# Kernel optimization log

Hardware: AMD Instinct MI355X
Metric: run time of the kernel (lower is better)

## Reference

```python
import jax, jax.numpy as jnp
import numpy as np

B, C, CI, H, W = 8, 256, 128, 64, 64
EPS = 1e-5

def conv1x1(x, w, b):
    # x: [B,C,H,W], w: [O,C], b: [O]
    return jnp.einsum('bchw,oc->bohw', x, w) + b[None, :, None, None]

def avgpool2(x):
    b, c, h, w = x.shape
    return x.reshape(b, c, h // 2, 2, w // 2, 2).mean(axis=(3, 5))

def setup_inputs() -> dict:
    key = jax.random.key(0)
    ks = jax.random.split(key, 16)
    s = lambda fan: 1.0 / np.sqrt(fan)
    inp = {
        'q': jax.random.normal(ks[0], (B, C, H, W), jnp.float32),
        'k': jax.random.normal(ks[1], (B, C, H, W), jnp.float32),
        'v': jax.random.normal(ks[2], (B, C, H, W), jnp.float32),
        'Wg':  jax.random.normal(ks[3], (CI, C), jnp.float32) * s(C),
        'bg':  jax.random.normal(ks[4], (CI,), jnp.float32) * s(C),
        'Wth': jax.random.normal(ks[5], (CI, C), jnp.float32) * s(C),
        'bth': jax.random.normal(ks[6], (CI,), jnp.float32) * s(C),
        'Wph': jax.random.normal(ks[7], (CI, C), jnp.float32) * s(C),
        'bph': jax.random.normal(ks[8], (CI,), jnp.float32) * s(C),
        'Ww':  jax.random.normal(ks[9], (C, CI), jnp.float32) * s(CI),
        'bw':  jax.random.normal(ks[10], (C,), jnp.float32) * s(CI),
        'gamma': jax.random.normal(ks[11], (C,), jnp.float32) * 0.1 + 1.0,
        'beta':  jax.random.normal(ks[12], (C,), jnp.float32) * 0.1,
        'mean':  jax.random.normal(ks[13], (C,), jnp.float32) * 0.1,
        'var':   jax.random.uniform(ks[14], (C,), jnp.float32, 0.5, 1.5),
    }
    return inp

def reference(q, k, v, Wg, bg, Wth, bth, Wph, bph, Ww, bw, gamma, beta, mean, var):
    b = q.shape[0]
    # g branch on v, phi branch on q: 1x1 conv then 2x2 avg-pool (sub_sample)
    g_x = avgpool2(conv1x1(v, Wg, bg)).reshape(b, CI, -1)            # [B,CI,M]
    g_x = g_x.transpose(0, 2, 1)                                      # [B,M,CI]
    theta_x = conv1x1(k, Wth, bth).reshape(b, CI, -1).transpose(0, 2, 1)  # [B,N,CI]
    phi_x = avgpool2(conv1x1(q, Wph, bph)).reshape(b, CI, -1)        # [B,CI,M]
    f = jnp.einsum('bnc,bcm->bnm', theta_x, phi_x)                   # [B,N,M]
    f_div_C = jax.nn.softmax(f, axis=-1)
    y = jnp.einsum('bnm,bmc->bnc', f_div_C, g_x)                     # [B,N,CI]
    y = y.transpose(0, 2, 1).reshape(b, CI, H, W)
    W_y = conv1x1(y, Ww, bw)
    # BatchNorm2d (inference form)
    W_y = (W_y - mean[None, :, None, None]) * (gamma[None, :, None, None]
            * jax.lax.rsqrt(var + EPS)[None, :, None, None]) + beta[None, :, None, None]
    return W_y + v
```

## Files before the change

kernel.cpp:

```cpp
#include <hip/hip_runtime.h>
#include <cstddef>

typedef unsigned short u16;
typedef unsigned int u32;
typedef __attribute__((ext_vector_type(8))) __bf16 bf16x8;
typedef __attribute__((ext_vector_type(4))) float f32x4;

constexpr int kB = 8, kC = 256, kCI = 128, kN = 4096, kM = 1024;
constexpr float kEPS = 1e-5f;

__device__ __forceinline__ u16 f2bf(float f) {
    u32 u = __float_as_uint(f);
    u32 r = (u + 0x7fffu + ((u >> 16) & 1u)) >> 16;
    return (u16)r;
}

__global__ __launch_bounds__(256) void prep_kernel(const float* __restrict__ Wth,
                                                   const float* __restrict__ Wph,
                                                   const float* __restrict__ Wg,
                                                   const float* __restrict__ Ww,
                                                   const float* __restrict__ bw,
                                                   const float* __restrict__ gamma,
                                                   const float* __restrict__ beta,
                                                   const float* __restrict__ mean,
                                                   const float* __restrict__ var,
                                                   u16* __restrict__ Wthb,
                                                   u16* __restrict__ Wphb,
                                                   u16* __restrict__ Wgb,
                                                   u16* __restrict__ Wwsb,
                                                   float* __restrict__ bb) {
    int idx = blockIdx.x * 256 + threadIdx.x;
    if (idx < 32768) {
        Wthb[idx] = f2bf(Wth[idx]);
    } else if (idx < 65536) {
        int j = idx - 32768; Wphb[j] = f2bf(Wph[j]);
    } else if (idx < 98304) {
        int j = idx - 65536; Wgb[j] = f2bf(Wg[j]);
    } else {
        int j = idx - 98304;
        int co = j >> 7;
        float sc = gamma[co] * rsqrtf(var[co] + kEPS);
        Wwsb[j] = f2bf(Ww[j] * sc);
        if ((j & 127) == 0) bb[co] = (bw[co] - mean[co]) * sc + beta[co];
    }
}

template <int CMAJOR, int POOL>
__global__ __launch_bounds__(256) void convp_kernel(const float* __restrict__ x,
                                                    const u16* __restrict__ Wb,
                                                    const float* __restrict__ bias,
                                                    u16* __restrict__ out, int Mn) {
    __shared__ __align__(16) u16 w_lds[128 * 72];
    __shared__ __align__(16) u16 x_lds[64 * 64];
    int t = threadIdx.x, b = blockIdx.y, n0 = blockIdx.x * 64;
    int w = t >> 6, lane = t & 63, l15 = lane & 15, quad = lane >> 4;
    int xn = t & 63, cbb = (t >> 6) * 2;

    f32x4 acc[8];
#pragma unroll
    for (int i = 0; i < 8; i++) acc[i] = (f32x4){0.f, 0.f, 0.f, 0.f};

    for (int c0 = 0; c0 < kC; c0 += 64) {
        __syncthreads();
#pragma unroll
        for (int i = 0; i < 4; i++) {
            int u = t + 256 * i;
            int ci = u >> 3, blk = u & 7;
            *(uint4*)&w_lds[ci * 72 + blk * 8] =
                *(const uint4*)&Wb[ci * kC + c0 + blk * 8];
        }
#pragma unroll
        for (int cc = 0; cc < 2; cc++) {
            int cb = cbb + cc;
            float f[8];
            if (POOL) {
                int p = n0 + xn, ph_ = p >> 5, pw_ = p & 31;
#pragma unroll
                for (int j = 0; j < 8; j++) {
                    const float* src = x + ((size_t)(b * kC + c0 + cb * 8 + j) * 64
                                            + 2 * ph_) * 64 + 2 * pw_;
                    float2 a = *(const float2*)src;
                    float2 b2 = *(const float2*)(src + 64);
                    f[j] = 0.25f * (a.x + a.y + b2.x + b2.y);
                }
            } else {
#pragma unroll
                for (int j = 0; j < 8; j++)
                    f[j] = x[(size_t)(b * kC + c0 + cb * 8 + j) * Mn + n0 + xn];
            }
            uint4 pk;
            pk.x = (u32)f2bf(f[0]) | ((u32)f2bf(f[1]) << 16);
            pk.y = (u32)f2bf(f[2]) | ((u32)f2bf(f[3]) << 16);
            pk.z = (u32)f2bf(f[4]) | ((u32)f2bf(f[5]) << 16);
            pk.w = (u32)f2bf(f[6]) | ((u32)f2bf(f[7]) << 16);
            *(uint4*)&x_lds[xn * 64 + ((cb ^ (xn & 7)) * 8)] = pk;
        }
        __syncthreads();

#pragma unroll
        for (int ks = 0; ks < 2; ks++) {
            int px = w * 16 + l15;
            bf16x8 xf = *(const bf16x8*)&x_lds[px * 64 + (((ks * 4 + quad) ^ (px & 7)) * 8)];
#pragma unroll
            for (int ct = 0; ct < 8; ct++) {
                bf16x8 wf = *(const bf16x8*)&w_lds[(ct * 16 + l15) * 72 + ks * 32 + quad * 8];
                if (CMAJOR)
                    acc[ct] = __builtin_amdgcn_mfma_f32_16x16x32_bf16(xf, wf, acc[ct], 0, 0, 0);
                else
                    acc[ct] = __builtin_amdgcn_mfma_f32_16x16x32_bf16(wf, xf, acc[ct], 0, 0, 0);
            }
        }
    }

    if (CMAJOR == 0) {
        int px = n0 + w * 16 + l15;
#pragma unroll
        for (int ct = 0; ct < 8; ct++) {
            int ci0 = ct * 16 + quad * 4;
            uint2 pk;
            pk.x = (u32)f2bf(acc[ct][0] + bias[ci0 + 0]) |
                   ((u32)f2bf(acc[ct][1] + bias[ci0 + 1]) << 16);
            pk.y = (u32)f2bf(acc[ct][2] + bias[ci0 + 2]) |
                   ((u32)f2bf(acc[ct][3] + bias[ci0 + 3]) << 16);
            *(uint2*)&out[(size_t)(b * Mn + px) * kCI + ci0] = pk;
        }
    } else {
        int px = n0 + w * 16 + quad * 4;
#pragma unroll
        for (int ct = 0; ct < 8; ct++) {
            int ci = ct * 16 + l15;
            float bs = bias[ci];
            uint2 pk;
            pk.x = (u32)f2bf(acc[ct][0] + bs) | ((u32)f2bf(acc[ct][1] + bs) << 16);
            pk.y = (u32)f2bf(acc[ct][2] + bs) | ((u32)f2bf(acc[ct][3] + bs) << 16);
            *(uint2*)&out[(size_t)(b * kCI + ci) * Mn + px] = pk;
        }
    }
}

__global__ __launch_bounds__(128) void attn_kernel(const u16* __restrict__ theta,
                                                   const u16* __restrict__ phi,
                                                   const u16* __restrict__ g,
                                                   u16* __restrict__ y) {
    __shared__ __align__(16) u16 ph_lds[8192];
    __shared__ __align__(16) u16 g_lds[8192];
    __shared__ __align__(16) u16 p_lds[4096];

    int t = threadIdx.x, b = blockIdx.y, n0 = blockIdx.x * 64;
    int w = t >> 6, lane = t & 63, l15 = lane & 15, quad = lane >> 4;

    bf16x8 thf[2][4];
    const u16* thB = theta + ((size_t)(b * kN) + n0 + w * 32) * kCI;
#pragma unroll
    for (int nt = 0; nt < 2; nt++)
#pragma unroll
        for (int ks = 0; ks < 4; ks++)
            thf[nt][ks] = *(const bf16x8*)&thB[(size_t)(nt * 16 + l15) * kCI + ks * 32 + quad * 8];

    f32x4 oacc[8][2];
#pragma unroll
    for (int ct = 0; ct < 8; ct++) {
        oacc[ct][0] = (f32x4){0.f, 0.f, 0.f, 0.f};
        oacc[ct][1] = (f32x4){0.f, 0.f, 0.f, 0.f};
    }
    float m_[2] = {-1e30f, -1e30f}, l_[2] = {0.f, 0.f};

    const u16* phB = phi + (size_t)b * kM * kCI;
    const u16* gB  = g   + (size_t)b * kCI * kM;
    u16* pw = p_lds + w * 2048;

    for (int c0 = 0; c0 < kM; c0 += 64) {
        __syncthreads();
#pragma unroll
        for (int it = 0; it < 8; it++) {
            int u = t + 128 * it;
            int row = u >> 4, cb = u & 15;
            *(uint4*)&ph_lds[(cb >> 2) * 2048 + row * 32 + (cb & 3) * 8] =
                *(const uint4*)&phB[(size_t)(c0 + row) * kCI + cb * 8];
        }
#pragma unroll
        for (int it = 0; it < 8; it++) {
            int u = t + 128 * it;
            int ci = u >> 3, mb = u & 7;
            *(uint4*)&g_lds[(mb >> 2) * 4096 + ci * 32 + (mb & 3) * 8] =
                *(const uint4*)&gB[(size_t)ci * kM + c0 + mb * 8];
        }
        __syncthreads();

        f32x4 sacc[4][2];
#pragma unroll
        for (int mt = 0; mt < 4; mt++) {
            sacc[mt][0] = (f32x4){0.f, 0.f, 0.f, 0.f};
            sacc[mt][1] = (f32x4){0.f, 0.f, 0.f, 0.f};
        }
#pragma unroll
        for (int ks = 0; ks < 4; ks++)
#pragma unroll
            for (int mt = 0; mt < 4; mt++) {
                bf16x8 a = *(const bf16x8*)&ph_lds[ks * 2048 + (mt * 16 + l15) * 32 + quad * 8];
                sacc[mt][0] = __builtin_amdgcn_mfma_f32_16x16x32_bf16(a, thf[0][ks], sacc[mt][0], 0, 0, 0);
                sacc[mt][1] = __builtin_amdgcn_mfma_f32_16x16x32_bf16(a, thf[1][ks], sacc[mt][1], 0, 0, 0);
            }

#pragma unroll
        for (int nt = 0; nt < 2; nt++) {
            float mc = -1e30f;
#pragma unroll
            for (int mt = 0; mt < 4; mt++)
#pragma unroll
                for (int r = 0; r < 4; r++) mc = fmaxf(mc, sacc[mt][nt][r]);
            mc = fmaxf(mc, __shfl_xor(mc, 16, 64));
            mc = fmaxf(mc, __shfl_xor(mc, 32, 64));
            float mp = m_[nt];
            float mn = fmaxf(mp, mc);
            int resc = __any(mn != mp);
            float alpha = __expf(mp - mn);
            m_[nt] = mn;
            float rs = 0.f;
#pragma unroll
            for (int mt = 0; mt < 4; mt++)
#pragma unroll
                for (int r = 0; r < 4; r++) {
                    float p = __expf(sacc[mt][nt][r] - mn);
                    sacc[mt][nt][r] = p;
                    rs += p;
                }
            rs += __shfl_xor(rs, 16, 64);
            rs += __shfl_xor(rs, 32, 64);
            l_[nt] = l_[nt] * alpha + rs;
            if (resc) {
#pragma unroll
                for (int ct = 0; ct < 8; ct++)
#pragma unroll
                    for (int r = 0; r < 4; r++) oacc[ct][nt][r] *= alpha;
            }
#pragma unroll
            for (int mt = 0; mt < 4; mt++)
#pragma unroll
                for (int h = 0; h < 2; h++) {
                    u32 ue = __float_as_uint(sacc[mt][nt][2 * h]) + 0x8000u;
                    u32 uo = __float_as_uint(sacc[mt][nt][2 * h + 1]) + 0x8000u;
                    u32 d = (ue >> 16) | (uo & 0xffff0000u);
                    int m = mt * 16 + quad * 4 + 2 * h;
                    int off = ((m >> 5) * 2 + nt) * 512 + (((m >> 3) & 3) * 16 + l15) * 8 + (m & 7);
                    *(u32*)&pw[off] = d;
                }
        }

#pragma unroll
        for (int ks2 = 0; ks2 < 2; ks2++) {
            bf16x8 b0 = *(const bf16x8*)&pw[(ks2 * 2 + 0) * 512 + (quad * 16 + l15) * 8];
            bf16x8 b1 = *(const bf16x8*)&pw[(ks2 * 2 + 1) * 512 + (quad * 16 + l15) * 8];
#pragma unroll
            for (int ct = 0; ct < 8; ct++) {
                bf16x8 a = *(const bf16x8*)&g_lds[ks2 * 4096 + (ct * 16 + l15) * 32 + quad * 8];
                oacc[ct][0] = __builtin_amdgcn_mfma_f32_16x16x32_bf16(a, b0, oacc[ct][0], 0, 0, 0);
                oacc[ct][1] = __builtin_amdgcn_mfma_f32_16x16x32_bf16(a, b1, oacc[ct][1], 0, 0, 0);
            }
        }
    }

#pragma unroll
    for (int nt = 0; nt < 2; nt++) {
        float inv = 1.0f / l_[nt];
        int n = n0 + w * 32 + nt * 16 + l15;
        u16* yr = y + ((size_t)(b * kN) + n) * kCI + quad * 4;
#pragma unroll
        for (int ct = 0; ct < 8; ct++) {
            uint2 pk;
            pk.x = (u32)f2bf(oacc[ct][nt][0] * inv) | ((u32)f2bf(oacc[ct][nt][1] * inv) << 16);
            pk.y = (u32)f2bf(oacc[ct][nt][2] * inv) | ((u32)f2bf(oacc[ct][nt][3] * inv) << 16);
            *(uint2*)&yr[ct * 16] = pk;
        }
    }
}

__global__ __launch_bounds__(256) void final_kernel(const u16* __restrict__ y,
                                                    const u16* __restrict__ Wws,
                                                    const float* __restrict__ bb,
                                                    const float* __restrict__ v,
                                                    float* __restrict__ out) {
    __shared__ __align__(16) u16 y_lds[64 * 136];
    int t = threadIdx.x, b = blockIdx.y, n0 = blockIdx.x * 64;
    int w = t >> 6, lane = t & 63, l15 = lane & 15, quad = lane >> 4;

#pragma unroll
    for (int i = 0; i < 4; i++) {
        int u = t + 256 * i;
        int row = u >> 4, blk = u & 15;
        *(uint4*)&y_lds[row * 136 + blk * 8] =
            *(const uint4*)&y[(size_t)(b * kN + n0 + row) * kCI + blk * 8];
    }
    __syncthreads();

    bf16x8 af[4];
#pragma unroll
    for (int ks = 0; ks < 4; ks++)
        af[ks] = *(const bf16x8*)&y_lds[(w * 16 + l15) * 136 + ks * 32 + quad * 8];

#pragma unroll
    for (int ct = 0; ct < 16; ct++) {
        f32x4 a = (f32x4){0.f, 0.f, 0.f, 0.f};
#pragma unroll
        for (int ks = 0; ks < 4; ks++) {
            bf16x8 bf = *(const bf16x8*)&Wws[(ct * 16 + l15) * kCI + ks * 32 + quad * 8];
            a = __builtin_amdgcn_mfma_f32_16x16x32_bf16(af[ks], bf, a, 0, 0, 0);
        }
        int co = ct * 16 + l15;
        float bbv = bb[co];
        size_t base = (size_t)(b * kC + co) * kN + n0 + w * 16 + quad * 4;
        float4 vv = *(const float4*)&v[base];
        float4 ov;
        ov.x = a[0] + bbv + vv.x;
        ov.y = a[1] + bbv + vv.y;
        ov.z = a[2] + bbv + vv.z;
        ov.w = a[3] + bbv + vv.w;
        *(float4*)&out[base] = ov;
    }
}

extern "C" void kernel_launch(void* const* d_in, const int* in_sizes, int n_in,
                              void* d_out, int out_size, void* d_ws, size_t ws_size,
                              hipStream_t stream) {
    (void)in_sizes; (void)n_in; (void)out_size; (void)ws_size;
    const float* q     = (const float*)d_in[0];
    const float* k     = (const float*)d_in[1];
    const float* v     = (const float*)d_in[2];
    const float* Wg    = (const float*)d_in[3];
    const float* bg    = (const float*)d_in[4];
    const float* Wth   = (const float*)d_in[5];
    const float* bth   = (const float*)d_in[6];
    const float* Wph   = (const float*)d_in[7];
    const float* bph   = (const float*)d_in[8];
    const float* Ww    = (const float*)d_in[9];
    const float* bw    = (const float*)d_in[10];
    const float* gamma = (const float*)d_in[11];
    const float* beta  = (const float*)d_in[12];
    const float* mean  = (const float*)d_in[13];
    const float* var   = (const float*)d_in[14];
    float* out = (float*)d_out;

    u16* wsu = (u16*)d_ws;
    u16*   theta = wsu;
    u16*   phi   = theta + 4194304;
    u16*   gbuf  = phi + 1048576;
    u16*   ybuf  = gbuf + 1048576;
    u16*   Wthb  = ybuf + 4194304;
    u16*   Wphb  = Wthb + 32768;
    u16*   Wgb   = Wphb + 32768;
    u16*   Wwsb  = Wgb + 32768;
    float* bbuf  = (float*)(Wwsb + 32768);

    prep_kernel<<<dim3(512), 256, 0, stream>>>(Wth, Wph, Wg, Ww, bw, gamma, beta,
                                               mean, var, Wthb, Wphb, Wgb, Wwsb, bbuf);
    convp_kernel<0, 0><<<dim3(64, 8), 256, 0, stream>>>(k, Wthb, bth, theta, kN);
    convp_kernel<0, 1><<<dim3(16, 8), 256, 0, stream>>>(q, Wphb, bph, phi, kM);
    convp_kernel<1, 1><<<dim3(16, 8), 256, 0, stream>>>(v, Wgb, bg, gbuf, kM);
    attn_kernel<<<dim3(64, 8), 128, 0, stream>>>(theta, phi, gbuf, ybuf);
    final_kernel<<<dim3(64, 8), 256, 0, stream>>>(ybuf, Wwsb, bbuf, v, out);
}
```

Measured before the change: 270.8 us.

## Merge conv launches, drop LDS staging in attention and final kernels

After: 260.3 us. 1.04x faster.

```diff
diff --git a/kernel.cpp b/kernel.cpp
--- a/kernel.cpp
+++ b/kernel.cpp
@@ -45,14 +45,14 @@
     }
 }
 
-template <int CMAJOR, int POOL>
-__global__ __launch_bounds__(256) void convp_kernel(const float* __restrict__ x,
-                                                    const u16* __restrict__ Wb,
-                                                    const float* __restrict__ bias,
-                                                    u16* __restrict__ out, int Mn) {
-    __shared__ __align__(16) u16 w_lds[128 * 72];
-    __shared__ __align__(16) u16 x_lds[64 * 64];
-    int t = threadIdx.x, b = blockIdx.y, n0 = blockIdx.x * 64;
+template <int POOL>
+__device__ __forceinline__ void conv_body(const float* __restrict__ x,
+                                          const u16* __restrict__ Wb,
+                                          const float* __restrict__ bias,
+                                          u16* __restrict__ out, int Mn,
+                                          int cmajor, int b, int n0,
+                                          u16* w_lds, u16* x_lds) {
+    int t = threadIdx.x;
     int w = t >> 6, lane = t & 63, l15 = lane & 15, quad = lane >> 4;
     int xn = t & 63, cbb = (t >> 6) * 2;
 
@@ -104,7 +104,7 @@
 #pragma unroll
             for (int ct = 0; ct < 8; ct++) {
                 bf16x8 wf = *(const bf16x8*)&w_lds[(ct * 16 + l15) * 72 + ks * 32 + quad * 8];
-                if (CMAJOR)
+                if (cmajor)
                     acc[ct] = __builtin_amdgcn_mfma_f32_16x16x32_bf16(xf, wf, acc[ct], 0, 0, 0);
                 else
                     acc[ct] = __builtin_amdgcn_mfma_f32_16x16x32_bf16(wf, xf, acc[ct], 0, 0, 0);
@@ -112,7 +112,7 @@
         }
     }
 
-    if (CMAJOR == 0) {
+    if (cmajor == 0) {
         int px = n0 + w * 16 + l15;
 #pragma unroll
         for (int ct = 0; ct < 8; ct++) {
@@ -138,19 +138,41 @@
     }
 }
 
-__global__ __launch_bounds__(128) void attn_kernel(const u16* __restrict__ theta,
-                                                   const u16* __restrict__ phi,
-                                                   const u16* __restrict__ g,
-                                                   u16* __restrict__ y) {
-    __shared__ __align__(16) u16 ph_lds[8192];
-    __shared__ __align__(16) u16 g_lds[8192];
-    __shared__ __align__(16) u16 p_lds[4096];
-
-    int t = threadIdx.x, b = blockIdx.y, n0 = blockIdx.x * 64;
-    int w = t >> 6, lane = t & 63, l15 = lane & 15, quad = lane >> 4;
+__global__ __launch_bounds__(256) void convs_kernel(const float* __restrict__ kin,
+                                                    const float* __restrict__ qin,
+                                                    const float* __restrict__ vin,
+                                                    const u16* __restrict__ Wthb,
+                                                    const u16* __restrict__ Wphb,
+                                                    const u16* __restrict__ Wgb,
+                                                    const float* __restrict__ bth,
+                                                    const float* __restrict__ bph,
+                                                    const float* __restrict__ bg,
+                                                    u16* __restrict__ theta,
+                                                    u16* __restrict__ phi,
+                                                    u16* __restrict__ g) {
+    __shared__ __align__(16) u16 w_lds[128 * 72];
+    __shared__ __align__(16) u16 x_lds[64 * 64];
+    int bx = blockIdx.x, b = blockIdx.y;
+    if (bx < 64)
+        conv_body<0>(kin, Wthb, bth, theta, kN, 0, b, bx * 64, w_lds, x_lds);
+    else if (bx < 80)
+        conv_body<1>(qin, Wphb, bph, phi, kM, 0, b, (bx - 64) * 64, w_lds, x_lds);
+    else
+        conv_body<1>(vin, Wgb, bg, g, kM, 1, b, (bx - 80) * 64, w_lds, x_lds);
+}
+
+__global__ __launch_bounds__(64, 1) void attn_kernel(const u16* __restrict__ theta,
+                                                     const u16* __restrict__ phi,
+                                                     const u16* __restrict__ g,
+                                                     u16* __restrict__ y) {
+    int b = blockIdx.y, n0 = blockIdx.x * 32;
+    int lane = threadIdx.x & 63, l15 = lane & 15, quad = lane >> 4;
+
+    const u16* phB = phi + (size_t)b * kM * kCI;
+    const u16* gB  = g   + (size_t)b * kCI * kM;
 
     bf16x8 thf[2][4];
-    const u16* thB = theta + ((size_t)(b * kN) + n0 + w * 32) * kCI;
+    const u16* thB = theta + ((size_t)(b * kN) + n0) * kCI;
 #pragma unroll
     for (int nt = 0; nt < 2; nt++)
 #pragma unroll
@@ -165,28 +187,14 @@
     }
     float m_[2] = {-1e30f, -1e30f}, l_[2] = {0.f, 0.f};
 
-    const u16* phB = phi + (size_t)b * kM * kCI;
-    const u16* gB  = g   + (size_t)b * kCI * kM;
-    u16* pw = p_lds + w * 2048;
-
     for (int c0 = 0; c0 < kM; c0 += 64) {
-        __syncthreads();
-#pragma unroll
-        for (int it = 0; it < 8; it++) {
-            int u = t + 128 * it;
-            int row = u >> 4, cb = u & 15;
-            *(uint4*)&ph_lds[(cb >> 2) * 2048 + row * 32 + (cb & 3) * 8] =
-                *(const uint4*)&phB[(size_t)(c0 + row) * kCI + cb * 8];
-        }
-#pragma unroll
-        for (int it = 0; it < 8; it++) {
-            int u = t + 128 * it;
-            int ci = u >> 3, mb = u & 7;
-            *(uint4*)&g_lds[(mb >> 2) * 4096 + ci * 32 + (mb & 3) * 8] =
-                *(const uint4*)&gB[(size_t)ci * kM + c0 + mb * 8];
-        }
-        __syncthreads();
-
+        bf16x8 pf[4][4];
+#pragma unroll
+        for (int mt = 0; mt < 4; mt++)
+#pragma unroll
+            for (int ks = 0; ks < 4; ks++)
+                pf[mt][ks] = *(const bf16x8*)&phB[(size_t)(c0 + mt * 16 + l15) * kCI +
+                                                  ks * 32 + quad * 8];
         f32x4 sacc[4][2];
 #pragma unroll
         for (int mt = 0; mt < 4; mt++) {
@@ -197,11 +205,13 @@
         for (int ks = 0; ks < 4; ks++)
 #pragma unroll
             for (int mt = 0; mt < 4; mt++) {
-                bf16x8 a = *(const bf16x8*)&ph_lds[ks * 2048 + (mt * 16 + l15) * 32 + quad * 8];
-                sacc[mt][0] = __builtin_amdgcn_mfma_f32_16x16x32_bf16(a, thf[0][ks], sacc[mt][0], 0, 0, 0);
-                sacc[mt][1] = __builtin_amdgcn_mfma_f32_16x16x32_bf16(a, thf[1][ks], sacc[mt][1], 0, 0, 0);
-            }
-
+                sacc[mt][0] = __builtin_amdgcn_mfma_f32_16x16x32_bf16(pf[mt][ks], thf[0][ks],
+                                                                      sacc[mt][0], 0, 0, 0);
+                sacc[mt][1] = __builtin_amdgcn_mfma_f32_16x16x32_bf16(pf[mt][ks], thf[1][ks],
+                                                                      sacc[mt][1], 0, 0, 0);
+            }
+
+        u32 d[2][4][2];
 #pragma unroll
         for (int nt = 0; nt < 2; nt++) {
             float mc = -1e30f;
@@ -211,10 +221,9 @@
                 for (int r = 0; r < 4; r++) mc = fmaxf(mc, sacc[mt][nt][r]);
             mc = fmaxf(mc, __shfl_xor(mc, 16, 64));
             mc = fmaxf(mc, __shfl_xor(mc, 32, 64));
-            float mp = m_[nt];
-            float mn = fmaxf(mp, mc);
-            int resc = __any(mn != mp);
-            float alpha = __expf(mp - mn);
+            float mn = fmaxf(m_[nt], mc);
+            int resc = __any(mn != m_[nt]);
+            float alpha = __expf(m_[nt] - mn);
             m_[nt] = mn;
             float rs = 0.f;
 #pragma unroll
@@ -237,25 +246,29 @@
 #pragma unroll
             for (int mt = 0; mt < 4; mt++)
 #pragma unroll
-                for (int h = 0; h < 2; h++) {
-                    u32 ue = __float_as_uint(sacc[mt][nt][2 * h]) + 0x8000u;
-                    u32 uo = __float_as_uint(sacc[mt][nt][2 * h + 1]) + 0x8000u;
-                    u32 d = (ue >> 16) | (uo & 0xffff0000u);
-                    int m = mt * 16 + quad * 4 + 2 * h;
-                    int off = ((m >> 5) * 2 + nt) * 512 + (((m >> 3) & 3) * 16 + l15) * 8 + (m & 7);
-                    *(u32*)&pw[off] = d;
+                for (int h = 0; h < 2; h++)
+                    d[nt][mt][h] = (u32)f2bf(sacc[mt][nt][2 * h]) |
+                                   ((u32)f2bf(sacc[mt][nt][2 * h + 1]) << 16);
+        }
+
+#pragma unroll
+        for (int ks2 = 0; ks2 < 2; ks2++) {
+            union { u32 u[4]; bf16x8 v; } bu[2];
+#pragma unroll
+            for (int nt = 0; nt < 2; nt++)
+#pragma unroll
+                for (int jj = 0; jj < 4; jj++) {
+                    int srcl = 16 * ((quad & 1) * 2 + (jj >> 1)) + l15;
+                    u32 va = (u32)__shfl((int)d[nt][ks2 * 2 + 0][jj & 1], srcl, 64);
+                    u32 vb = (u32)__shfl((int)d[nt][ks2 * 2 + 1][jj & 1], srcl, 64);
+                    bu[nt].u[jj] = (quad >> 1) ? vb : va;
                 }
-        }
-
-#pragma unroll
-        for (int ks2 = 0; ks2 < 2; ks2++) {
-            bf16x8 b0 = *(const bf16x8*)&pw[(ks2 * 2 + 0) * 512 + (quad * 16 + l15) * 8];
-            bf16x8 b1 = *(const bf16x8*)&pw[(ks2 * 2 + 1) * 512 + (quad * 16 + l15) * 8];
 #pragma unroll
             for (int ct = 0; ct < 8; ct++) {
-                bf16x8 a = *(const bf16x8*)&g_lds[ks2 * 4096 + (ct * 16 + l15) * 32 + quad * 8];
-                oacc[ct][0] = __builtin_amdgcn_mfma_f32_16x16x32_bf16(a, b0, oacc[ct][0], 0, 0, 0);
-                oacc[ct][1] = __builtin_amdgcn_mfma_f32_16x16x32_bf16(a, b1, oacc[ct][1], 0, 0, 0);
+                bf16x8 a = *(const bf16x8*)&gB[(size_t)(ct * 16 + l15) * kM + c0 +
+                                               ks2 * 32 + quad * 8];
+                oacc[ct][0] = __builtin_amdgcn_mfma_f32_16x16x32_bf16(a, bu[0].v, oacc[ct][0], 0, 0, 0);
+                oacc[ct][1] = __builtin_amdgcn_mfma_f32_16x16x32_bf16(a, bu[1].v, oacc[ct][1], 0, 0, 0);
             }
         }
     }
@@ -263,7 +276,7 @@
 #pragma unroll
     for (int nt = 0; nt < 2; nt++) {
         float inv = 1.0f / l_[nt];
-        int n = n0 + w * 32 + nt * 16 + l15;
+        int n = n0 + nt * 16 + l15;
         u16* yr = y + ((size_t)(b * kN) + n) * kCI + quad * 4;
 #pragma unroll
         for (int ct = 0; ct < 8; ct++) {
@@ -275,28 +288,18 @@
     }
 }
 
-__global__ __launch_bounds__(256) void final_kernel(const u16* __restrict__ y,
-                                                    const u16* __restrict__ Wws,
-                                                    const float* __restrict__ bb,
-                                                    const float* __restrict__ v,
-                                                    float* __restrict__ out) {
-    __shared__ __align__(16) u16 y_lds[64 * 136];
-    int t = threadIdx.x, b = blockIdx.y, n0 = blockIdx.x * 64;
-    int w = t >> 6, lane = t & 63, l15 = lane & 15, quad = lane >> 4;
-
-#pragma unroll
-    for (int i = 0; i < 4; i++) {
-        int u = t + 256 * i;
-        int row = u >> 4, blk = u & 15;
-        *(uint4*)&y_lds[row * 136 + blk * 8] =
-            *(const uint4*)&y[(size_t)(b * kN + n0 + row) * kCI + blk * 8];
-    }
-    __syncthreads();
+__global__ __launch_bounds__(64, 1) void final_kernel(const u16* __restrict__ y,
+                                                      const u16* __restrict__ Wws,
+                                                      const float* __restrict__ bb,
+                                                      const float* __restrict__ v,
+                                                      float* __restrict__ out) {
+    int b = blockIdx.y, n0 = blockIdx.x * 16;
+    int lane = threadIdx.x & 63, l15 = lane & 15, quad = lane >> 4;
 
     bf16x8 af[4];
 #pragma unroll
     for (int ks = 0; ks < 4; ks++)
-        af[ks] = *(const bf16x8*)&y_lds[(w * 16 + l15) * 136 + ks * 32 + quad * 8];
+        af[ks] = *(const bf16x8*)&y[(size_t)(b * kN + n0 + l15) * kCI + ks * 32 + quad * 8];
 
 #pragma unroll
     for (int ct = 0; ct < 16; ct++) {
@@ -308,7 +311,7 @@
         }
         int co = ct * 16 + l15;
         float bbv = bb[co];
-        size_t base = (size_t)(b * kC + co) * kN + n0 + w * 16 + quad * 4;
+        size_t base = (size_t)(b * kC + co) * kN + n0 + quad * 4;
         float4 vv = *(const float4*)&v[base];
         float4 ov;
         ov.x = a[0] + bbv + vv.x;
@@ -353,9 +356,8 @@
 
     prep_kernel<<<dim3(512), 256, 0, stream>>>(Wth, Wph, Wg, Ww, bw, gamma, beta,
                                                mean, var, Wthb, Wphb, Wgb, Wwsb, bbuf);
-    convp_kernel<0, 0><<<dim3(64, 8), 256, 0, stream>>>(k, Wthb, bth, theta, kN);
-    convp_kernel<0, 1><<<dim3(16, 8), 256, 0, stream>>>(q, Wphb, bph, phi, kM);
-    convp_kernel<1, 1><<<dim3(16, 8), 256, 0, stream>>>(v, Wgb, bg, gbuf, kM);
-    attn_kernel<<<dim3(64, 8), 128, 0, stream>>>(theta, phi, gbuf, ybuf);
-    final_kernel<<<dim3(64, 8), 256, 0, stream>>>(ybuf, Wwsb, bbuf, v, out);
-}
+    convs_kernel<<<dim3(96, 8), 256, 0, stream>>>(k, q, v, Wthb, Wphb, Wgb,
+                                                  bth, bph, bg, theta, phi, gbuf);
+    attn_kernel<<<dim3(128, 8), 64, 0, stream>>>(theta, phi, gbuf, ybuf);
+    final_kernel<<<dim3(256, 8), 64, 0, stream>>>(ybuf, Wwsb, bbuf, v, out);
+}
```
